# Kernel tuning notes

Hardware: AMD Instinct MI355X
Metric: run time of the kernel (lower is better)

## Reference

```python
import jax, jax.numpy as jnp
import numpy as np

IN_FEATURES = 4096
OUT_FEATURES = 4096
BATCH = 4096
MAX_STATES = 100.0
THRESHOLD = MAX_STATES * 0.2  # 20.0


def setup_inputs() -> dict:
    key = jax.random.key(0)
    k1, k2 = jax.random.split(key)
    spike_input = jax.random.uniform(k1, (BATCH, IN_FEATURES), dtype=jnp.float32)
    # synapse_states ~ N(0,1)*20 + threshold, clamped to [-max, max] (as in __init__)
    states = jax.random.normal(k2, (OUT_FEATURES, IN_FEATURES), dtype=jnp.float32) * 20.0 + THRESHOLD
    synapse_states = jnp.clip(states, -MAX_STATES, MAX_STATES)
    membrane_potential = jnp.zeros((OUT_FEATURES,), dtype=jnp.float32)
    adaptive_threshold = jnp.full((OUT_FEATURES,), 2.0, dtype=jnp.float32)
    refractory_count = jnp.zeros((OUT_FEATURES,), dtype=jnp.float32)
    return {
        "spike_input": spike_input,
        "synapse_states": synapse_states,
        "membrane_potential": membrane_potential,
        "adaptive_threshold": adaptive_threshold,
        "refractory_count": refractory_count,
    }


def reference(spike_input, synapse_states, membrane_potential, adaptive_threshold, refractory_count):
    # Ternary weights: +1 if state > thr, -1 if state < -thr, else 0
    w = jnp.where(synapse_states > THRESHOLD, 1.0,
                  jnp.where(synapse_states < -THRESHOLD, -1.0, 0.0)).astype(spike_input.dtype)
    # current: [B, out] = x [B, in] @ w.T [in, out]
    current = jnp.einsum('bi,oi->bo', spike_input, w)
    is_refractory = (refractory_count > 0).astype(current.dtype)[None, :]  # [1, out]
    effective_current = current * (1.0 - is_refractory)
    new_v_mem = membrane_potential[None, :] * 0.5 + effective_current      # [B, out]
    spikes = (new_v_mem >= adaptive_threshold[None, :]).astype(current.dtype)
    return spikes
```

## Files before the change

### kernel.cpp

```cpp
#include <hip/hip_runtime.h>


#define K_DIM 4096
#define N_OUT 4096
#define B_DIM 4096

typedef __attribute__((ext_vector_type(4))) int i32x4;
typedef __attribute__((ext_vector_type(4))) float float4v;

__global__ __launch_bounds__(256) void prep_kernel(
    const float* __restrict__ X, const float* __restrict__ S,
    char* __restrict__ Xq, char* __restrict__ Wq)
{
    const int tid = blockIdx.x * 256 + threadIdx.x;
    const float4v* __restrict__ X4 = (const float4v*)X;
    const float4v* __restrict__ S4 = (const float4v*)S;
    union { char c[16]; i32x4 v; } xo, wo;
#pragma unroll
    for (int g = 0; g < 4; ++g) {
        float4v x = X4[(size_t)tid * 4 + g];
        float4v s = S4[(size_t)tid * 4 + g];
#pragma unroll
        for (int j = 0; j < 4; ++j) {
            xo.c[g * 4 + j] = (char)(int)(x[j] * 127.0f + 0.5f);
            wo.c[g * 4 + j] = (s[j] > 20.0f) ? (char)1
                            : ((s[j] < -20.0f) ? (char)-1 : (char)0);
        }
    }
    ((i32x4*)Xq)[tid] = xo.v;
    ((i32x4*)Wq)[tid] = wo.v;
}

__global__ __launch_bounds__(256) void snn_gemm(
    const char* __restrict__ Xq,
    const char* __restrict__ Wq,
    const float* __restrict__ vmem,
    const float* __restrict__ thr,
    const float* __restrict__ refr,
    float* __restrict__ out)
{
    __shared__ char As[128 * 64];
    __shared__ char Bs[128 * 64];

    const int t = threadIdx.x;
    const int lane = t & 63;
    const int wave = t >> 6;
    const int wr = wave >> 1;
    const int wc = wave & 1;
    const int fr = lane & 15;
    const int fq = lane >> 4;

    const int bm = blockIdx.x * 128;
    const int bn = blockIdx.y * 128;

    i32x4 acc[4][4] = {};

    const int e0 = t * 16;
    const int e1 = (256 + t) * 16;
    const int row0 = e0 >> 6, c0 = e0 & 63;
    const int row1 = e1 >> 6, c1 = e1 & 63;

    const char* gA0 = Xq + (size_t)(bm + row0) * K_DIM + c0;
    const char* gA1 = Xq + (size_t)(bm + row1) * K_DIM + c1;
    const char* gB0 = Wq + (size_t)(bn + row0) * K_DIM + c0;
    const char* gB1 = Wq + (size_t)(bn + row1) * K_DIM + c1;

    for (int kt = 0; kt < K_DIM; kt += 64) {
        __builtin_amdgcn_global_load_lds(
            (const __attribute__((address_space(1))) void*)(gA0 + kt),
            (__attribute__((address_space(3))) void*)(As + e0), 16, 0, 0);
        __builtin_amdgcn_global_load_lds(
            (const __attribute__((address_space(1))) void*)(gA1 + kt),
            (__attribute__((address_space(3))) void*)(As + e1), 16, 0, 0);
        __builtin_amdgcn_global_load_lds(
            (const __attribute__((address_space(1))) void*)(gB0 + kt),
            (__attribute__((address_space(3))) void*)(Bs + e0), 16, 0, 0);
        __builtin_amdgcn_global_load_lds(
            (const __attribute__((address_space(1))) void*)(gB1 + kt),
            (__attribute__((address_space(3))) void*)(Bs + e1), 16, 0, 0);
        __syncthreads();

        i32x4 a[4], b[4];
#pragma unroll
        for (int m = 0; m < 4; ++m)
            a[m] = *(const i32x4*)(As + (wr * 64 + m * 16 + fr) * 64 + fq * 16);
#pragma unroll
        for (int n = 0; n < 4; ++n)
            b[n] = *(const i32x4*)(Bs + (wc * 64 + n * 16 + fr) * 64 + fq * 16);

#pragma unroll
        for (int m = 0; m < 4; ++m)
#pragma unroll
            for (int n = 0; n < 4; ++n)
                acc[m][n] = __builtin_amdgcn_mfma_i32_16x16x64_i8(
                    a[m], b[n], acc[m][n], 0, 0, 0);

        __syncthreads();
    }

    const float inv127 = 1.0f / 127.0f;
#pragma unroll
    for (int n = 0; n < 4; ++n) {
        const int gc = bn + wc * 64 + n * 16 + fr;
        const bool refract = refr[gc] > 0.0f;
        const float tv = thr[gc];
        const float vm = vmem[gc] * 0.5f;
#pragma unroll
        for (int m = 0; m < 4; ++m) {
            const int gr = bm + wr * 64 + m * 16 + fq * 4;
#pragma unroll
            for (int j = 0; j < 4; ++j) {
                const float cur = refract ? 0.0f : (float)acc[m][n][j] * inv127;
                const float v = vm + cur;
                out[(size_t)(gr + j) * N_OUT + gc] = (v >= tv) ? 1.0f : 0.0f;
            }
        }
    }
}

extern "C" void kernel_launch(void* const* d_in, const int* in_sizes, int n_in,
                              void* d_out, int out_size, void* d_ws, size_t ws_size,
                              hipStream_t stream) {
    const float* X    = (const float*)d_in[0];
    const float* S    = (const float*)d_in[1];
    const float* vmem = (const float*)d_in[2];
    const float* thr  = (const float*)d_in[3];
    const float* refr = (const float*)d_in[4];
    float* out = (float*)d_out;

    char* Xq = (char*)d_ws;
    char* Wq = (char*)d_ws + (size_t)B_DIM * K_DIM;

    prep_kernel<<<(B_DIM * K_DIM) / 16 / 256, 256, 0, stream>>>(X, S, Xq, Wq);

    dim3 grid(B_DIM / 128, N_OUT / 128);
    snn_gemm<<<grid, 256, 0, stream>>>(Xq, Wq, vmem, thr, refr, out);
}
```

Baseline: 270.1 us.

## Rewrite int8 GEMM with 256x256 tiles, 4-stage LDS pipeline and swizzle

Replaces the 128x128 single-buffered GEMM with a 256x256 tile kernel using 8 waves. It adds a 4-deep LDS ring buffer loaded with global_load_lds and explicit vmcnt waits, an XOR swizzle against LDS bank conflicts, and setprio around the MFMA blocks. The goal is to hide global load latency behind compute and raise arithmetic intensity per tile. In exchange it uses 128KB of dynamic LDS per block, which limits occupancy, and depends on hand-counted waitcnt/barrier correctness.

```diff
diff --git a/kernel.cpp b/kernel.cpp
--- a/kernel.cpp
+++ b/kernel.cpp
@@ -4,9 +4,13 @@
 #define K_DIM 4096
 #define N_OUT 4096
 #define B_DIM 4096
+#define BK 64
 
 typedef __attribute__((ext_vector_type(4))) int i32x4;
 typedef __attribute__((ext_vector_type(4))) float float4v;
+
+#define AS1 __attribute__((address_space(1)))
+#define AS3 __attribute__((address_space(3)))
 
 __global__ __launch_bounds__(256) void prep_kernel(
     const float* __restrict__ X, const float* __restrict__ S,
@@ -31,7 +35,57 @@
     ((i32x4*)Wq)[tid] = wo.v;
 }
 
-__global__ __launch_bounds__(256) void snn_gemm(
+
+#define STAGE2(SBUF, KTS, PH) do {                                            \
+    if ((PH) == 0) {                                                          \
+        __builtin_amdgcn_global_load_lds((const AS1 void*)(pA0 + (KTS)),      \
+            (AS3 void*)(lds + (SBUF) * 32768 + dst0), 16, 0, 0);              \
+        __builtin_amdgcn_global_load_lds((const AS1 void*)(pA1 + (KTS)),      \
+            (AS3 void*)(lds + (SBUF) * 32768 + dst1), 16, 0, 0);              \
+    } else {                                                                  \
+        __builtin_amdgcn_global_load_lds((const AS1 void*)(pB0 + (KTS)),      \
+            (AS3 void*)(lds + (SBUF) * 32768 + 16384 + dst0), 16, 0, 0);      \
+        __builtin_amdgcn_global_load_lds((const AS1 void*)(pB1 + (KTS)),      \
+            (AS3 void*)(lds + (SBUF) * 32768 + 16384 + dst1), 16, 0, 0);      \
+    } } while (0)
+
+#define ITER(RBUF, SBUF, DO_STAGE, WAITN) do {                                \
+    const char* base = lds + (RBUF) * 32768;                                  \
+    i32x4 a[4], b[4];                                                         \
+    _Pragma("unroll")                                                         \
+    for (int n = 0; n < 4; ++n) b[n] = *(const i32x4*)(base + sB + n * 1024); \
+    _Pragma("unroll")                                                         \
+    for (int m = 0; m < 4; ++m) a[m] = *(const i32x4*)(base + sA + m * 1024); \
+    if (DO_STAGE) STAGE2(SBUF, kts, 0);                                       \
+    asm volatile("s_barrier" ::: "memory");                                   \
+    __builtin_amdgcn_s_setprio(1);                                            \
+    _Pragma("unroll")                                                         \
+    for (int m = 0; m < 4; ++m)                                               \
+        _Pragma("unroll")                                                     \
+        for (int n = 0; n < 4; ++n)                                           \
+            acc[m][n] = __builtin_amdgcn_mfma_i32_16x16x64_i8(                \
+                a[m], b[n], acc[m][n], 0, 0, 0);                              \
+    __builtin_amdgcn_s_setprio(0);                                            \
+    asm volatile("s_barrier" ::: "memory");                                   \
+    _Pragma("unroll")                                                         \
+    for (int m = 0; m < 4; ++m)                                               \
+        a[m] = *(const i32x4*)(base + sA + 4096 + m * 1024);                  \
+    if (DO_STAGE) STAGE2(SBUF, kts, 1);                                       \
+    asm volatile("s_barrier" ::: "memory");                                   \
+    __builtin_amdgcn_s_setprio(1);                                            \
+    _Pragma("unroll")                                                         \
+    for (int m = 0; m < 4; ++m)                                               \
+        _Pragma("unroll")                                                     \
+        for (int n = 0; n < 4; ++n)                                           \
+            acc[m + 4][n] = __builtin_amdgcn_mfma_i32_16x16x64_i8(            \
+                a[m], b[n], acc[m + 4][n], 0, 0, 0);                          \
+    __builtin_amdgcn_s_setprio(0);                                            \
+    asm volatile("s_waitcnt vmcnt(" #WAITN ")" ::: "memory");                 \
+    asm volatile("s_barrier" ::: "memory");                                   \
+    kts += BK;                                                                \
+} while (0)
+
+__global__ __launch_bounds__(512, 2) void snn_gemm8(
     const char* __restrict__ Xq,
     const char* __restrict__ Wq,
     const float* __restrict__ vmem,
@@ -39,80 +93,74 @@
     const float* __restrict__ refr,
     float* __restrict__ out)
 {
-    __shared__ char As[128 * 64];
-    __shared__ char Bs[128 * 64];
+    extern __shared__ char lds[];
 
-    const int t = threadIdx.x;
-    const int lane = t & 63;
-    const int wave = t >> 6;
-    const int wr = wave >> 1;
-    const int wc = wave & 1;
-    const int fr = lane & 15;
-    const int fq = lane >> 4;
+    const int tid  = threadIdx.x;
+    const int lane = tid & 63;
+    const int wid  = tid >> 6;
+    const int wr   = wid >> 2;
+    const int wcol = wid & 3;
+    const int fr   = lane & 15;
+    const int fq   = lane >> 4;
 
-    const int bm = blockIdx.x * 128;
-    const int bn = blockIdx.y * 128;
+    const int bm = blockIdx.x * 256;
+    const int bn = blockIdx.y * 256;
 
-    i32x4 acc[4][4] = {};
+    const int swz16 = (fq ^ (fr & 3)) << 4;
+    const int sA = wr * 8192 + fr * 64 + swz16;
+    const int sB = 16384 + wcol * 4096 + fr * 64 + swz16;
 
-    const int e0 = t * 16;
-    const int e1 = (256 + t) * 16;
-    const int row0 = e0 >> 6, c0 = e0 & 63;
-    const int row1 = e1 >> 6, c1 = e1 & 63;
+    int rowS[2], colS[2];
+#pragma unroll
+    for (int r = 0; r < 2; ++r) {
+        int o  = (r * 512 + tid) * 16;
+        int os = o ^ (((o >> 6) & 3) << 4);
+        rowS[r] = os >> 6;
+        colS[r] = os & 63;
+    }
+    const char* pA0 = Xq + (size_t)(bm + rowS[0]) * K_DIM + colS[0];
+    const char* pA1 = Xq + (size_t)(bm + rowS[1]) * K_DIM + colS[1];
+    const char* pB0 = Wq + (size_t)(bn + rowS[0]) * K_DIM + colS[0];
+    const char* pB1 = Wq + (size_t)(bn + rowS[1]) * K_DIM + colS[1];
+    const int dst0 = tid * 16;
+    const int dst1 = tid * 16 + 8192;
 
-    const char* gA0 = Xq + (size_t)(bm + row0) * K_DIM + c0;
-    const char* gA1 = Xq + (size_t)(bm + row1) * K_DIM + c1;
-    const char* gB0 = Wq + (size_t)(bn + row0) * K_DIM + c0;
-    const char* gB1 = Wq + (size_t)(bn + row1) * K_DIM + c1;
+    i32x4 acc[8][4] = {};
 
-    for (int kt = 0; kt < K_DIM; kt += 64) {
-        __builtin_amdgcn_global_load_lds(
-            (const __attribute__((address_space(1))) void*)(gA0 + kt),
-            (__attribute__((address_space(3))) void*)(As + e0), 16, 0, 0);
-        __builtin_amdgcn_global_load_lds(
-            (const __attribute__((address_space(1))) void*)(gA1 + kt),
-            (__attribute__((address_space(3))) void*)(As + e1), 16, 0, 0);
-        __builtin_amdgcn_global_load_lds(
-            (const __attribute__((address_space(1))) void*)(gB0 + kt),
-            (__attribute__((address_space(3))) void*)(Bs + e0), 16, 0, 0);
-        __builtin_amdgcn_global_load_lds(
-            (const __attribute__((address_space(1))) void*)(gB1 + kt),
-            (__attribute__((address_space(3))) void*)(Bs + e1), 16, 0, 0);
-        __syncthreads();
+    STAGE2(0, 0, 0);   STAGE2(0, 0, 1);
+    STAGE2(1, 64, 0);  STAGE2(1, 64, 1);
+    STAGE2(2, 128, 0); STAGE2(2, 128, 1);
+    asm volatile("s_waitcnt vmcnt(8)" ::: "memory");
+    asm volatile("s_barrier" ::: "memory");
 
-        i32x4 a[4], b[4];
-#pragma unroll
-        for (int m = 0; m < 4; ++m)
-            a[m] = *(const i32x4*)(As + (wr * 64 + m * 16 + fr) * 64 + fq * 16);
-#pragma unroll
-        for (int n = 0; n < 4; ++n)
-            b[n] = *(const i32x4*)(Bs + (wc * 64 + n * 16 + fr) * 64 + fq * 16);
+    int kts = 192;
 
-#pragma unroll
-        for (int m = 0; m < 4; ++m)
-#pragma unroll
-            for (int n = 0; n < 4; ++n)
-                acc[m][n] = __builtin_amdgcn_mfma_i32_16x16x64_i8(
-                    a[m], b[n], acc[m][n], 0, 0, 0);
-
-        __syncthreads();
+#pragma unroll 1
+    for (int tt = 0; tt < 15; ++tt) {
+        ITER(0, 3, 1, 8);
+        ITER(1, 0, 1, 8);
+        ITER(2, 1, 1, 8);
+        ITER(3, 2, 1, 8);
     }
+    ITER(0, 3, 1, 8);
+    ITER(1, 0, 0, 4);
+    ITER(2, 0, 0, 0);
+    ITER(3, 0, 0, 0);
 
     const float inv127 = 1.0f / 127.0f;
 #pragma unroll
     for (int n = 0; n < 4; ++n) {
-        const int gc = bn + wc * 64 + n * 16 + fr;
+        const int gc = bn + wcol * 64 + n * 16 + fr;
         const bool refract = refr[gc] > 0.0f;
         const float tv = thr[gc];
         const float vm = vmem[gc] * 0.5f;
 #pragma unroll
-        for (int m = 0; m < 4; ++m) {
-            const int gr = bm + wr * 64 + m * 16 + fq * 4;
+        for (int m = 0; m < 8; ++m) {
+            const int gr = bm + wr * 128 + m * 16 + fq * 4;
 #pragma unroll
             for (int j = 0; j < 4; ++j) {
                 const float cur = refract ? 0.0f : (float)acc[m][n][j] * inv127;
-                const float v = vm + cur;
-                out[(size_t)(gr + j) * N_OUT + gc] = (v >= tv) ? 1.0f : 0.0f;
+                out[(size_t)(gr + j) * N_OUT + gc] = (vm + cur >= tv) ? 1.0f : 0.0f;
             }
         }
     }
@@ -133,6 +181,8 @@
 
     prep_kernel<<<(B_DIM * K_DIM) / 16 / 256, 256, 0, stream>>>(X, S, Xq, Wq);
 
-    dim3 grid(B_DIM / 128, N_OUT / 128);
-    snn_gemm<<<grid, 256, 0, stream>>>(Xq, Wq, vmem, thr, refr, out);
+    hipFuncSetAttribute((const void*)snn_gemm8,
+                        hipFuncAttributeMaxDynamicSharedMemorySize, 131072);
+    dim3 grid(B_DIM / 256, N_OUT / 256);
+    snn_gemm8<<<grid, 512, 131072, stream>>>(Xq, Wq, vmem, thr, refr, out);
 }
```

Result: faster. 242.7 us (-10.2%).
